# Kernel optimization log

Hardware: AMD Instinct MI355X
Metric: run time of the kernel (lower is better)

The kernel has to match this reference:

```python
import jax, jax.numpy as jnp
import numpy as np

EPS = 1e-06


def setup_inputs() -> dict:
    key = jax.random.key(0)
    k1, k2 = jax.random.split(key)
    x = jax.random.normal(k1, (256, 4096), dtype=jnp.float32)
    # learned parameter, init matches torch.randn(...) * 0.1
    shapelets = jax.random.normal(k2, (8, 16, 128), dtype=jnp.float32) * 0.1
    return {"x": x, "shapelets": shapelets}


def reference(x, shapelets):
    B, T = x.shape
    C, Kc, L = shapelets.shape
    nwin = T - L + 1  # stride-1 unfold

    # sliding windows: [B, nwin, L] (same materialization as torch unfold)
    idx = jnp.arange(nwin)[:, None] + jnp.arange(L)[None, :]
    x_win = x[:, idx]

    # z-normalize each window (population std, unbiased=False)
    mu_x = jnp.mean(x_win, axis=2, keepdims=True)
    var_x = jnp.mean((x_win - mu_x) ** 2, axis=2, keepdims=True)
    std_x = jnp.sqrt(var_x) + EPS
    x_norm = (x_win - mu_x) / std_x

    # z-normalize shapelets per class/shapelet
    mu_s = jnp.mean(shapelets, axis=2, keepdims=True)
    var_s = jnp.mean((shapelets - mu_s) ** 2, axis=2, keepdims=True)
    std_s = jnp.sqrt(var_s) + EPS
    s_norm = (shapelets - mu_s) / std_s

    # normalized cross-correlation: [B, nwin, C, Kc]
    corr = jnp.einsum('btl,ckl->btck', x_norm, s_norm) / L

    # max over window positions, concat classes -> [B, C*Kc]
    max_vals = jnp.max(corr, axis=1)  # [B, C, Kc]
    return max_vals.reshape(B, C * Kc)
```

## Files before the change

kernel.cpp:

```cpp
#include <hip/hip_runtime.h>
#include <hip/hip_bf16.h>

typedef __attribute__((ext_vector_type(8))) short short8;
typedef __attribute__((ext_vector_type(16))) float f32x16;

#define T_LEN 4096
#define L_LEN 128
#define NWIN  3969
#define CK    128

__device__ __forceinline__ unsigned short f2bf(float f) {
    unsigned u = __float_as_uint(f);
    u += 0x7fffu + ((u >> 16) & 1u);
    return (unsigned short)(u >> 16);
}

__global__ void prep_sh(const float* __restrict__ sh,
                        unsigned short* __restrict__ wsB) {
    const int ck = blockIdx.x;
    const int l  = threadIdx.x;
    __shared__ float rs[2], rq[2];
    const int lane = l & 63, wv = l >> 6;

    float v = sh[ck * L_LEN + l];
    float s = v, q = v * v;
    #pragma unroll
    for (int off = 32; off >= 1; off >>= 1) {
        s += __shfl_xor(s, off);
        q += __shfl_xor(q, off);
    }
    if (lane == 0) { rs[wv] = s; rq[wv] = q; }
    __syncthreads();
    float sm = rs[0] + rs[1], sq = rq[0] + rq[1];
    float mu  = sm * (1.f / L_LEN);
    float var = fmaxf(sq * (1.f / L_LEN) - mu * mu, 0.f);
    float inv = 1.f / (sqrtf(var) + 1e-6f);
    unsigned short b = f2bf((v - mu) * inv);
    const int nt = ck >> 5, n = ck & 31;
    const int kt = l >> 4, hi = (l >> 3) & 1, j = l & 7;
    wsB[((((nt * 8 + kt) * 64) + hi * 32 + n) << 3) + j] = b;
}

__global__ __launch_bounds__(512, 2)
void conv_row(const float* __restrict__ x,
              const unsigned short* __restrict__ wsB,
              float* __restrict__ out) {
    __shared__ alignas(16) unsigned short xb[8][T_LEN];
    __shared__ float sty[T_LEN];
    __shared__ float PSs[513], PQs[513];
    __shared__ float grpS[8], grpQ[8];
    __shared__ float wmax[8][CK];

    const int tid  = threadIdx.x;
    const int lane = tid & 63;
    const int wv   = tid >> 6;
    const int row  = blockIdx.x;
    const float4* xr4 = (const float4*)(x + row * T_LEN);

    short8 Bf[4][8];
    {
        const short8* Bp = (const short8*)wsB;
        #pragma unroll
        for (int nt = 0; nt < 4; ++nt)
            #pragma unroll
            for (int kt = 0; kt < 8; ++kt)
                Bf[nt][kt] = Bp[(nt * 8 + kt) * 64 + lane];
    }

    float v[16];
    {
        float4 a0 = xr4[2 * tid];
        float4 a1 = xr4[2 * tid + 1];
        float4 a2 = make_float4(0.f, 0.f, 0.f, 0.f), a3 = a2;
        if (tid < 511) { a2 = xr4[2 * tid + 2]; a3 = xr4[2 * tid + 3]; }
        v[0]=a0.x; v[1]=a0.y; v[2]=a0.z;  v[3]=a0.w;
        v[4]=a1.x; v[5]=a1.y; v[6]=a1.z;  v[7]=a1.w;
        v[8]=a2.x; v[9]=a2.y; v[10]=a2.z; v[11]=a2.w;
        v[12]=a3.x; v[13]=a3.y; v[14]=a3.z; v[15]=a3.w;
    }
    unsigned short bb[16];
    #pragma unroll
    for (int i = 0; i < 16; ++i) bb[i] = f2bf(v[i]);
    #pragma unroll
    for (int c = 0; c < 8; ++c) {
        short8 w8;
        #pragma unroll
        for (int j = 0; j < 8; ++j) w8[j] = (short)bb[c + j];
        *(short8*)&xb[c][8 * tid] = w8;
    }

    float s = 0.f, q = 0.f;
    #pragma unroll
    for (int i = 0; i < 8; ++i) { s += v[i]; q += v[i] * v[i]; }
    float is = s, iq = q;
    #pragma unroll
    for (int off = 1; off < 64; off <<= 1) {
        float ts = __shfl_up(is, off);
        float tq = __shfl_up(iq, off);
        if (lane >= off) { is += ts; iq += tq; }
    }
    if (lane == 63) { grpS[wv] = is; grpQ[wv] = iq; }
    __syncthreads();
    float os = 0.f, oq = 0.f;
    #pragma unroll
    for (int w = 0; w < 7; ++w) if (w < wv) { os += grpS[w]; oq += grpQ[w]; }
    PSs[tid] = os + is - s;
    PQs[tid] = oq + iq - q;
    if (tid == 511) { PSs[512] = os + is; PQs[512] = oq + iq; }
    __syncthreads();

    if (tid < 497) {
        float S = PSs[tid + 16] - PSs[tid];
        float Q = PQs[tid + 16] - PQs[tid];
        float4 b0 = make_float4(0.f, 0.f, 0.f, 0.f), b1 = b0;
        if (tid <= 495) { b0 = xr4[2 * tid + 32]; b1 = xr4[2 * tid + 33]; }
        float xn[8] = {b0.x, b0.y, b0.z, b0.w, b1.x, b1.y, b1.z, b1.w};
        #pragma unroll
        for (int e = 0; e < 8; ++e) {
            int w = 8 * tid + e;
            if (w < NWIN) {
                float mu  = S * (1.f / L_LEN);
                float var = fmaxf(Q * (1.f / L_LEN) - mu * mu, 0.f);
                float sd  = sqrtf(var) + 1e-6f;
                sty[w] = 1.f / (sd * (float)L_LEN);
                S += xn[e] - v[e];
                Q += xn[e] * xn[e] - v[e] * v[e];
            }
        }
    }
    __syncthreads();

    const int hi  = lane >> 5;
    const int m32 = lane & 31;
    float vmax[4];
    #pragma unroll
    for (int nt = 0; nt < 4; ++nt) vmax[nt] = -1e30f;

    #pragma unroll 1
    for (int ii = 0; ii < 16; ++ii) {
        const int ci = (ii + 2 * wv) & 15;
        const int T0 = (ci < 15) ? ci * 256 : (NWIN - 256);
        const int e0 = T0 + wv;
        const int c  = e0 & 7;
        const int B0 = e0 >> 3;

        float sr[16];
        #pragma unroll
        for (int r = 0; r < 16; ++r)
            sr[r] = sty[e0 + 32 * hi + 8 * (r & 3) + 64 * (r >> 2)];

        const unsigned short* ab = &xb[c][8 * (B0 + m32 + hi)];

        #pragma unroll
        for (int h = 0; h < 2; ++h) {
            f32x16 a0, a1;
            #pragma unroll
            for (int r = 0; r < 16; ++r) { a0[r] = 0.f; a1[r] = 0.f; }

            __builtin_amdgcn_s_setprio(1);
            #pragma unroll
            for (int kt = 0; kt < 8; ++kt) {
                short8 af = *(const short8*)(ab + 16 * kt);
                a0 = __builtin_amdgcn_mfma_f32_32x32x16_bf16(
                    af, Bf[2 * h][kt], a0, 0, 0, 0);
                a1 = __builtin_amdgcn_mfma_f32_32x32x16_bf16(
                    af, Bf[2 * h + 1][kt], a1, 0, 0, 0);
            }
            __builtin_amdgcn_s_setprio(0);

            float v0 = vmax[2 * h], v1 = vmax[2 * h + 1];
            #pragma unroll
            for (int r = 0; r < 16; ++r) {
                v0 = fmaxf(v0, a0[r] * sr[r]);
                v1 = fmaxf(v1, a1[r] * sr[r]);
            }
            vmax[2 * h] = v0; vmax[2 * h + 1] = v1;
        }
    }

    #pragma unroll
    for (int nt = 0; nt < 4; ++nt) {
        float vx = fmaxf(vmax[nt], __shfl_xor(vmax[nt], 32));
        if (lane < 32) wmax[wv][nt * 32 + m32] = vx;
    }
    __syncthreads();
    if (tid < CK) {
        float m = wmax[0][tid];
        #pragma unroll
        for (int w = 1; w < 8; ++w) m = fmaxf(m, wmax[w][tid]);
        out[row * CK + tid] = m;
    }
}

extern "C" void kernel_launch(void* const* d_in, const int* in_sizes, int n_in,
                              void* d_out, int out_size, void* d_ws, size_t ws_size,
                              hipStream_t stream) {
    (void)in_sizes; (void)n_in; (void)out_size; (void)ws_size;
    const float* x  = (const float*)d_in[0];
    const float* sh = (const float*)d_in[1];
    unsigned short* wsB = (unsigned short*)d_ws;
    float* out = (float*)d_out;

    prep_sh<<<128, 128, 0, stream>>>(sh, wsB);
    conv_row<<<256, 512, 0, stream>>>(x, wsB, out);
}
```

Before: 85.76 us.

## Split shapelet columns across wave pairs using 1024-thread blocks

Doubles the block to 1024 threads. Each pair of waves now shares the same window positions, and each wave handles half of the 128 shapelet columns, so it keeps half as many B fragments in registers and runs one MFMA pass per tile instead of two. The prefix-sum and window-statistics setup is rescaled so each thread handles 4 elements instead of 8, and the final max reduction is remapped across the 16 waves. The aim is more waves in flight per CU to hide LDS and MFMA latency. The cost is a larger block with more barrier participants, and LDS use limits blocks per CU, so with 256 rows on 256 CUs concurrency may change little.

```diff
diff --git a/kernel.cpp b/kernel.cpp
--- a/kernel.cpp
+++ b/kernel.cpp
@@ -1,6 +1,7 @@
 #include <hip/hip_runtime.h>
 #include <hip/hip_bf16.h>
 
+typedef __attribute__((ext_vector_type(4))) short short4v;
 typedef __attribute__((ext_vector_type(8))) short short8;
 typedef __attribute__((ext_vector_type(16))) float f32x16;
 
@@ -41,57 +42,58 @@
     wsB[((((nt * 8 + kt) * 64) + hi * 32 + n) << 3) + j] = b;
 }
 
-__global__ __launch_bounds__(512, 2)
+__global__ __launch_bounds__(1024, 4)
 void conv_row(const float* __restrict__ x,
               const unsigned short* __restrict__ wsB,
               float* __restrict__ out) {
     __shared__ alignas(16) unsigned short xb[8][T_LEN];
     __shared__ float sty[T_LEN];
-    __shared__ float PSs[513], PQs[513];
-    __shared__ float grpS[8], grpQ[8];
-    __shared__ float wmax[8][CK];
+    __shared__ float PSs[1025], PQs[1025];
+    __shared__ float grpS[16], grpQ[16];
+    __shared__ float wmax[16][64];
 
     const int tid  = threadIdx.x;
     const int lane = tid & 63;
     const int wv   = tid >> 6;
+    const int wg   = wv >> 1;
+    const int wh   = wv & 1;
     const int row  = blockIdx.x;
     const float4* xr4 = (const float4*)(x + row * T_LEN);
 
-    short8 Bf[4][8];
+    short8 Bf[2][8];
     {
         const short8* Bp = (const short8*)wsB;
         #pragma unroll
-        for (int nt = 0; nt < 4; ++nt)
+        for (int nt = 0; nt < 2; ++nt)
             #pragma unroll
             for (int kt = 0; kt < 8; ++kt)
-                Bf[nt][kt] = Bp[(nt * 8 + kt) * 64 + lane];
-    }
-
-    float v[16];
+                Bf[nt][kt] = Bp[((2 * wh + nt) * 8 + kt) * 64 + lane];
+    }
+
+    float v[12];
     {
-        float4 a0 = xr4[2 * tid];
-        float4 a1 = xr4[2 * tid + 1];
-        float4 a2 = make_float4(0.f, 0.f, 0.f, 0.f), a3 = a2;
-        if (tid < 511) { a2 = xr4[2 * tid + 2]; a3 = xr4[2 * tid + 3]; }
+        float4 a0 = xr4[tid];
+        float4 a1 = make_float4(0.f, 0.f, 0.f, 0.f), a2 = a1;
+        if (tid < 1023) a1 = xr4[tid + 1];
+        if (tid < 1022) a2 = xr4[tid + 2];
         v[0]=a0.x; v[1]=a0.y; v[2]=a0.z;  v[3]=a0.w;
         v[4]=a1.x; v[5]=a1.y; v[6]=a1.z;  v[7]=a1.w;
         v[8]=a2.x; v[9]=a2.y; v[10]=a2.z; v[11]=a2.w;
-        v[12]=a3.x; v[13]=a3.y; v[14]=a3.z; v[15]=a3.w;
-    }
-    unsigned short bb[16];
-    #pragma unroll
-    for (int i = 0; i < 16; ++i) bb[i] = f2bf(v[i]);
+    }
+    unsigned short bb[12];
+    #pragma unroll
+    for (int i = 0; i < 12; ++i) bb[i] = f2bf(v[i]);
     #pragma unroll
     for (int c = 0; c < 8; ++c) {
-        short8 w8;
-        #pragma unroll
-        for (int j = 0; j < 8; ++j) w8[j] = (short)bb[c + j];
-        *(short8*)&xb[c][8 * tid] = w8;
+        short4v w4;
+        #pragma unroll
+        for (int j = 0; j < 4; ++j) w4[j] = (short)bb[c + j];
+        *(short4v*)&xb[c][4 * tid] = w4;
     }
 
     float s = 0.f, q = 0.f;
     #pragma unroll
-    for (int i = 0; i < 8; ++i) { s += v[i]; q += v[i] * v[i]; }
+    for (int i = 0; i < 4; ++i) { s += v[i]; q += v[i] * v[i]; }
     float is = s, iq = q;
     #pragma unroll
     for (int off = 1; off < 64; off <<= 1) {
@@ -103,21 +105,21 @@
     __syncthreads();
     float os = 0.f, oq = 0.f;
     #pragma unroll
-    for (int w = 0; w < 7; ++w) if (w < wv) { os += grpS[w]; oq += grpQ[w]; }
+    for (int w = 0; w < 15; ++w) if (w < wv) { os += grpS[w]; oq += grpQ[w]; }
     PSs[tid] = os + is - s;
     PQs[tid] = oq + iq - q;
-    if (tid == 511) { PSs[512] = os + is; PQs[512] = oq + iq; }
-    __syncthreads();
-
-    if (tid < 497) {
-        float S = PSs[tid + 16] - PSs[tid];
-        float Q = PQs[tid + 16] - PQs[tid];
-        float4 b0 = make_float4(0.f, 0.f, 0.f, 0.f), b1 = b0;
-        if (tid <= 495) { b0 = xr4[2 * tid + 32]; b1 = xr4[2 * tid + 33]; }
-        float xn[8] = {b0.x, b0.y, b0.z, b0.w, b1.x, b1.y, b1.z, b1.w};
-        #pragma unroll
-        for (int e = 0; e < 8; ++e) {
-            int w = 8 * tid + e;
+    if (tid == 1023) { PSs[1024] = os + is; PQs[1024] = oq + iq; }
+    __syncthreads();
+
+    if (tid <= 992) {
+        float S = PSs[tid + 32] - PSs[tid];
+        float Q = PQs[tid + 32] - PQs[tid];
+        float4 b0 = make_float4(0.f, 0.f, 0.f, 0.f);
+        if (tid < 992) b0 = xr4[tid + 32];
+        float xn[4] = {b0.x, b0.y, b0.z, b0.w};
+        #pragma unroll
+        for (int e = 0; e < 4; ++e) {
+            int w = 4 * tid + e;
             if (w < NWIN) {
                 float mu  = S * (1.f / L_LEN);
                 float var = fmaxf(Q * (1.f / L_LEN) - mu * mu, 0.f);
@@ -132,15 +134,13 @@
 
     const int hi  = lane >> 5;
     const int m32 = lane & 31;
-    float vmax[4];
-    #pragma unroll
-    for (int nt = 0; nt < 4; ++nt) vmax[nt] = -1e30f;
+    float vmax0 = -1e30f, vmax1 = -1e30f;
 
     #pragma unroll 1
     for (int ii = 0; ii < 16; ++ii) {
-        const int ci = (ii + 2 * wv) & 15;
+        const int ci = (ii + 2 * wg) & 15;
         const int T0 = (ci < 15) ? ci * 256 : (NWIN - 256);
-        const int e0 = T0 + wv;
+        const int e0 = T0 + wg;
         const int c  = e0 & 7;
         const int B0 = e0 >> 3;
 
@@ -151,43 +151,41 @@
 
         const unsigned short* ab = &xb[c][8 * (B0 + m32 + hi)];
 
-        #pragma unroll
-        for (int h = 0; h < 2; ++h) {
-            f32x16 a0, a1;
-            #pragma unroll
-            for (int r = 0; r < 16; ++r) { a0[r] = 0.f; a1[r] = 0.f; }
-
-            __builtin_amdgcn_s_setprio(1);
-            #pragma unroll
-            for (int kt = 0; kt < 8; ++kt) {
-                short8 af = *(const short8*)(ab + 16 * kt);
-                a0 = __builtin_amdgcn_mfma_f32_32x32x16_bf16(
-                    af, Bf[2 * h][kt], a0, 0, 0, 0);
-                a1 = __builtin_amdgcn_mfma_f32_32x32x16_bf16(
-                    af, Bf[2 * h + 1][kt], a1, 0, 0, 0);
-            }
-            __builtin_amdgcn_s_setprio(0);
-
-            float v0 = vmax[2 * h], v1 = vmax[2 * h + 1];
-            #pragma unroll
-            for (int r = 0; r < 16; ++r) {
-                v0 = fmaxf(v0, a0[r] * sr[r]);
-                v1 = fmaxf(v1, a1[r] * sr[r]);
-            }
-            vmax[2 * h] = v0; vmax[2 * h + 1] = v1;
+        f32x16 a0, a1;
+        #pragma unroll
+        for (int r = 0; r < 16; ++r) { a0[r] = 0.f; a1[r] = 0.f; }
+
+        __builtin_amdgcn_s_setprio(1);
+        #pragma unroll
+        for (int kt = 0; kt < 8; ++kt) {
+            short8 af = *(const short8*)(ab + 16 * kt);
+            a0 = __builtin_amdgcn_mfma_f32_32x32x16_bf16(
+                af, Bf[0][kt], a0, 0, 0, 0);
+            a1 = __builtin_amdgcn_mfma_f32_32x32x16_bf16(
+                af, Bf[1][kt], a1, 0, 0, 0);
         }
-    }
-
-    #pragma unroll
-    for (int nt = 0; nt < 4; ++nt) {
-        float vx = fmaxf(vmax[nt], __shfl_xor(vmax[nt], 32));
-        if (lane < 32) wmax[wv][nt * 32 + m32] = vx;
+        __builtin_amdgcn_s_setprio(0);
+
+        #pragma unroll
+        for (int r = 0; r < 16; ++r) {
+            vmax0 = fmaxf(vmax0, a0[r] * sr[r]);
+            vmax1 = fmaxf(vmax1, a1[r] * sr[r]);
+        }
+    }
+
+    {
+        float v0 = fmaxf(vmax0, __shfl_xor(vmax0, 32));
+        float v1 = fmaxf(vmax1, __shfl_xor(vmax1, 32));
+        if (lane < 32) { wmax[wv][m32] = v0; wmax[wv][32 + m32] = v1; }
     }
     __syncthreads();
     if (tid < CK) {
-        float m = wmax[0][tid];
-        #pragma unroll
-        for (int w = 1; w < 8; ++w) m = fmaxf(m, wmax[w][tid]);
+        const int ntg = tid >> 5, n = tid & 31;
+        const int whs = ntg >> 1, j = ntg & 1;
+        float m = -1e30f;
+        #pragma unroll
+        for (int g = 0; g < 8; ++g)
+            m = fmaxf(m, wmax[g * 2 + whs][j * 32 + n]);
         out[row * CK + tid] = m;
     }
 }
@@ -202,5 +200,5 @@
     float* out = (float*)d_out;
 
     prep_sh<<<128, 128, 0, stream>>>(sh, wsB);
-    conv_row<<<256, 512, 0, stream>>>(x, wsB, out);
-}
+    conv_row<<<256, 1024, 0, stream>>>(x, wsB, out);
+}
```

Measured after the change: 84.57 us. No clear change (-1.4%).
